# Optimization experiments

Measured on AMD Instinct MI355X. Metric: run time of the kernel, lower is better.

Reference implementation:

```python
import jax, jax.numpy as jnp
import numpy as np

# --- Mamba2Enc config (matches init_kwargs + mamba_ssm Mamba2 defaults) ---
D_IN = 1024
D_MODEL = 512
N_CLASSES = 2
NLAYERS = 2
D_STATE = 64
D_CONV = 4
EXPAND = 2
HEADDIM = 64
D_INNER = EXPAND * D_MODEL            # 1024
NHEADS = D_INNER // HEADDIM           # 16
CONV_DIM = D_INNER + 2 * D_STATE      # 1152 (ngroups=1)
D_IN_PROJ = 2 * D_INNER + 2 * D_STATE + NHEADS  # 2192
EPS = 1e-5


def setup_inputs() -> dict:
    key = jax.random.key(0)
    ks = jax.random.split(key, 10)
    def w(k, shape, sc=0.02):
        return jax.random.normal(k, shape, jnp.float32) * sc
    x = jax.random.normal(ks[0], (4, 4096, D_IN), jnp.float32)
    # fc1
    W1 = w(ks[1], (D_MODEL, D_IN))
    b1 = jnp.zeros((D_MODEL,), jnp.float32)
    # per-layer params stacked on leading NLAYERS axis
    ln_w = jnp.ones((NLAYERS, D_MODEL), jnp.float32)
    ln_b = jnp.zeros((NLAYERS, D_MODEL), jnp.float32)
    W_in = w(ks[2], (NLAYERS, D_IN_PROJ, D_MODEL))
    conv_w = w(ks[3], (NLAYERS, CONV_DIM, D_CONV), 0.1)
    conv_b = jnp.zeros((NLAYERS, CONV_DIM), jnp.float32)
    # dt_bias so that softplus(dt_bias) ~ [0.001, 0.1] (mamba init range)
    dt_bias = jax.random.uniform(ks[4], (NLAYERS, NHEADS), jnp.float32, -6.0, -2.3)
    A_log = jnp.log(jnp.tile(jnp.arange(1, NHEADS + 1, dtype=jnp.float32), (NLAYERS, 1)))
    Dskip = jnp.ones((NLAYERS, NHEADS), jnp.float32)
    norm_w = jnp.ones((NLAYERS, D_INNER), jnp.float32)
    W_out = w(ks[5], (NLAYERS, D_MODEL, D_INNER))
    # classifier
    Wc = w(ks[6], (N_CLASSES, D_MODEL))
    bc = jnp.zeros((N_CLASSES,), jnp.float32)
    return dict(x=x, W1=W1, b1=b1, ln_w=ln_w, ln_b=ln_b, W_in=W_in,
                conv_w=conv_w, conv_b=conv_b, dt_bias=dt_bias, A_log=A_log,
                Dskip=Dskip, norm_w=norm_w, W_out=W_out, Wc=Wc, bc=bc)


def _layernorm(h, w, b):
    mu = jnp.mean(h, axis=-1, keepdims=True)
    var = jnp.mean(jnp.square(h - mu), axis=-1, keepdims=True)
    return (h - mu) * jax.lax.rsqrt(var + EPS) * w + b


def _silu(x):
    return x * jax.nn.sigmoid(x)


def _mamba2(x, W_in, conv_w, conv_b, dt_bias, A_log, Dskip, norm_w, W_out):
    b, l, _ = x.shape
    zxbcdt = jnp.einsum('bld,ed->ble', x, W_in)  # (b, l, D_IN_PROJ)
    z = zxbcdt[..., :D_INNER]
    xBC = zxbcdt[..., D_INNER:D_INNER + CONV_DIM]
    dt = jax.nn.softplus(zxbcdt[..., -NHEADS:] + dt_bias)  # (b, l, h)
    # causal depthwise conv1d (kernel D_CONV) + silu
    xp = jnp.pad(xBC, ((0, 0), (D_CONV - 1, 0), (0, 0)))
    xBC = sum(xp[:, k:k + l, :] * conv_w[:, k] for k in range(D_CONV)) + conv_b
    xBC = _silu(xBC)
    xh = xBC[..., :D_INNER].reshape(b, l, NHEADS, HEADDIM)
    B = xBC[..., D_INNER:D_INNER + D_STATE]   # (b, l, n) ngroups=1
    C = xBC[..., D_INNER + D_STATE:]          # (b, l, n)
    A = -jnp.exp(A_log)                       # (h,)
    dA = jnp.exp(dt * A)                      # (b, l, h)
    dtx = dt[..., None] * xh                  # (b, l, h, p)

    def step(hstate, inp):
        dA_t, dtx_t, B_t, C_t = inp  # (b,h), (b,h,p), (b,n), (b,n)
        hstate = hstate * dA_t[:, :, None, None] + dtx_t[:, :, None, :] * B_t[:, None, :, None]
        y = jnp.einsum('bn,bhnp->bhp', C_t, hstate)
        return hstate, y

    init = jnp.zeros((b, NHEADS, D_STATE, HEADDIM), x.dtype)
    xs = (dA.transpose(1, 0, 2), dtx.transpose(1, 0, 2, 3),
          B.transpose(1, 0, 2), C.transpose(1, 0, 2))
    _, ys = jax.lax.scan(step, init, xs)      # ys: (l, b, h, p)
    y = ys.transpose(1, 0, 2, 3) + Dskip[None, None, :, None] * xh
    y = y.reshape(b, l, D_INNER)
    # RMSNormGated (norm_before_gate=False): rmsnorm(y * silu(z)) * weight
    y = y * _silu(z)
    y = y * jax.lax.rsqrt(jnp.mean(jnp.square(y), axis=-1, keepdims=True) + EPS) * norm_w
    return jnp.einsum('ble,de->bld', y, W_out)


def reference(x, W1, b1, ln_w, ln_b, W_in, conv_w, conv_b, dt_bias, A_log,
              Dskip, norm_w, W_out, Wc, bc):
    # fc1: Linear + GELU (dropout is identity at eval)
    h = jax.nn.gelu(jnp.einsum('bli,di->bld', x, W1) + b1, approximate=False)
    for i in range(NLAYERS):
        h = h + _mamba2(_layernorm(h, ln_w[i], ln_b[i]), W_in[i], conv_w[i],
                        conv_b[i], dt_bias[i], A_log[i], Dskip[i], norm_w[i], W_out[i])
    return jnp.einsum('bld,cd->blc', h, Wc) + bc
```

## Files before the change

kernel.cpp:

```cpp
#include <hip/hip_runtime.h>
#include <hip/hip_bf16.h>
#include <math.h>

#define BATCH 4
#define SEQ 4096
#define ROWS 16384
#define DIN 1024
#define DMODEL 512
#define DINNER 1024
#define DSTATE 64
#define NH 16
#define HD 64
#define CONVDIM 1152
#define DPROJ 2192
#define NPAD 2304
#define QC 64
#define NCH 64
#define LD 72

typedef __attribute__((ext_vector_type(8))) __bf16 bf16x8;
typedef __attribute__((ext_vector_type(4))) __bf16 bf16x4;
typedef __attribute__((ext_vector_type(4))) float f32x4;

__device__ __forceinline__ float siluf(float x){ return x / (1.f + __expf(-x)); }
__device__ __forceinline__ float geluf(float x){ return 0.5f*x*(1.f + erff(x*0.70710678118654752440f)); }

__device__ __forceinline__ bf16x8 scale8(bf16x8 v, float s){
  bf16x8 r;
  #pragma unroll
  for (int e = 0; e < 8; e++) r[e] = (__bf16)((float)v[e]*s);
  return r;
}

__global__ void cast_bf16_kernel(const float* __restrict__ src, __bf16* __restrict__ dst, long n){
  long i = (long)blockIdx.x*blockDim.x + threadIdx.x;
  long stride = (long)gridDim.x*blockDim.x;
  for (; i < n; i += stride) dst[i] = (__bf16)src[i];
}

__global__ void pad_win_kernel(const float* __restrict__ src, __bf16* __restrict__ dst){
  long total = 2L*NPAD*DMODEL;
  long i = (long)blockIdx.x*blockDim.x + threadIdx.x;
  long stride = (long)gridDim.x*blockDim.x;
  for (; i < total; i += stride){
    int k = (int)(i % DMODEL);
    int n = (int)((i / DMODEL) % NPAD);
    int l = (int)(i / ((long)DMODEL*NPAD));
    float v = (n < DPROJ) ? src[((long)l*DPROJ + n)*DMODEL + k] : 0.f;
    dst[i] = (__bf16)v;
  }
}

template<typename OutT, int EPI>
__global__ __launch_bounds__(256) void gemm_bt(const __bf16* __restrict__ A, const __bf16* __restrict__ Bm,
                                               OutT* __restrict__ C, const float* __restrict__ bias,
                                               int K, int Nc){
  __shared__ __align__(16) __bf16 As[128*32];
  __shared__ __align__(16) __bf16 Bs[128*32];
  int bm = blockIdx.x, bn = blockIdx.y;
  int tid = threadIdx.x;
  int lane = tid & 63, wid = tid >> 6;
  int wm = (wid >> 1)*64, wn = (wid & 1)*64;
  int lr = lane & 15, kb = lane >> 4;
  f32x4 acc[4][4] = {};
  const char* Ab = (const char*)A + (size_t)bm*128*(size_t)(K*2);
  const char* Bb = (const char*)Bm + (size_t)bn*128*(size_t)(K*2);
  int nkk = K >> 5;
  for (int kk = 0; kk < nkk; kk++){
    #pragma unroll
    for (int it = 0; it < 2; it++){
      int off = it*4096 + tid*16;
      int row = off >> 6, cb = off & 63;
      *(int4*)((char*)As + off) = *(const int4*)(Ab + (size_t)row*(K*2) + kk*64 + cb);
      *(int4*)((char*)Bs + off) = *(const int4*)(Bb + (size_t)row*(K*2) + kk*64 + cb);
    }
    __syncthreads();
    bf16x8 af[4], bfr[4];
    #pragma unroll
    for (int mi = 0; mi < 4; mi++) af[mi] = *(const bf16x8*)(As + (wm + mi*16 + lr)*32 + kb*8);
    #pragma unroll
    for (int ni = 0; ni < 4; ni++) bfr[ni] = *(const bf16x8*)(Bs + (wn + ni*16 + lr)*32 + kb*8);
    #pragma unroll
    for (int mi = 0; mi < 4; mi++)
      #pragma unroll
      for (int ni = 0; ni < 4; ni++)
        acc[mi][ni] = __builtin_amdgcn_mfma_f32_16x16x32_bf16(af[mi], bfr[ni], acc[mi][ni], 0, 0, 0);
    __syncthreads();
  }
  #pragma unroll
  for (int mi = 0; mi < 4; mi++){
    #pragma unroll
    for (int ni = 0; ni < 4; ni++){
      int r0 = bm*128 + wm + mi*16 + (lane >> 4)*4;
      int c  = bn*128 + wn + ni*16 + lr;
      if (c < Nc){
        OutT* Cp = C + (size_t)r0*Nc + c;
        #pragma unroll
        for (int j = 0; j < 4; j++){
          float v = acc[mi][ni][j];
          if (EPI == 1){ float u = v + bias[c]; v = geluf(u); }
          if (EPI == 2){ v += (float)Cp[(size_t)j*Nc]; }
          Cp[(size_t)j*Nc] = (OutT)v;
        }
      }
    }
  }
}

__global__ __launch_bounds__(256) void ln_kernel(const float* __restrict__ h, const float* __restrict__ w,
                                                 const float* __restrict__ b, __bf16* __restrict__ out){
  int row = blockIdx.x*4 + (threadIdx.x >> 6);
  int lane = threadIdx.x & 63;
  const float* hr = h + (size_t)row*DMODEL + lane*8;
  float4 a = *(const float4*)hr, a2 = *(const float4*)(hr+4);
  float v[8] = {a.x,a.y,a.z,a.w,a2.x,a2.y,a2.z,a2.w};
  float s = 0.f;
  #pragma unroll
  for (int i = 0; i < 8; i++) s += v[i];
  #pragma unroll
  for (int o = 32; o; o >>= 1) s += __shfl_xor(s, o, 64);
  float mu = s*(1.f/512.f);
  float q = 0.f;
  #pragma unroll
  for (int i = 0; i < 8; i++){ float d = v[i]-mu; q += d*d; }
  #pragma unroll
  for (int o = 32; o; o >>= 1) q += __shfl_xor(q, o, 64);
  float rs = rsqrtf(q*(1.f/512.f) + 1e-5f);
  const float* wp = w + lane*8; const float* bp = b + lane*8;
  bf16x8 o8;
  #pragma unroll
  for (int i = 0; i < 8; i++) o8[i] = (__bf16)((v[i]-mu)*rs*wp[i] + bp[i]);
  *(bf16x8*)(out + (size_t)row*DMODEL + lane*8) = o8;
}

__global__ __launch_bounds__(256) void conv_bc(const __bf16* __restrict__ zx, const float* __restrict__ cw,
                                               const float* __restrict__ cb, float* __restrict__ BCc){
  int idx = blockIdx.x*256 + threadIdx.x;
  int j = idx & 127;
  long bt = idx >> 7;
  int t = (int)(bt & (SEQ-1));
  int ch = DINNER + j;
  const __bf16* src = zx + (size_t)bt*DPROJ + 2048 + j;
  float acc = cb[ch] + (float)src[0]*cw[ch*4+3];
  if (t >= 1) acc += (float)src[-1L*DPROJ]*cw[ch*4+2];
  if (t >= 2) acc += (float)src[-2L*DPROJ]*cw[ch*4+1];
  if (t >= 3) acc += (float)src[-3L*DPROJ]*cw[ch*4+0];
  BCc[idx] = siluf(acc);
}

__global__ __launch_bounds__(256) void dt_kernel(const __bf16* __restrict__ zx, const float* __restrict__ dt_bias,
                                                 float* __restrict__ dtb){
  int idx = blockIdx.x*256 + threadIdx.x;
  int hh = idx & (NH-1); long bt = idx >> 4;
  float v = (float)zx[(size_t)bt*DPROJ + (DPROJ-NH) + hh] + dt_bias[hh];
  dtb[idx] = (v > 20.f) ? v : log1pf(__expf(v));
}

__global__ __launch_bounds__(64) void ssd_state(const __bf16* __restrict__ zx, const float* __restrict__ BCc,
                                                const float* __restrict__ dtb, const float* __restrict__ A_log,
                                                const float* __restrict__ cw, const float* __restrict__ cb,
                                                __bf16* __restrict__ Schunk, float* __restrict__ Pbuf){
  __shared__ __align__(16) __bf16 Bt[64*LD];
  __shared__ __align__(16) __bf16 Xt[64*LD];
  int c = blockIdx.x, h = blockIdx.y, b = blockIdx.z;
  int lane = threadIdx.x;
  int lr = lane & 15, kb = lane >> 4, hi4 = lane >> 4;
  long t0 = (long)c*QC;
  size_t bt0 = (size_t)b*SEQ + t0;
  int bh = b*NH + h;
  float Ac = -expf(A_log[h]);
  float dtv = dtb[(bt0 + lane)*NH + h];
  float cum = dtv*Ac;
  #pragma unroll
  for (int off = 1; off < 64; off <<= 1){ float v = __shfl_up(cum, off, 64); if (lane >= off) cum += v; }
  float cumQ = __shfl(cum, 63, 64);
  float w = __expf(cumQ - cum) * dtv;
  {
    const float* bp = BCc + bt0*128 + lane;
    for (int tb = 0; tb < 8; tb++){
      bf16x8 buf;
      #pragma unroll
      for (int u = 0; u < 8; u++){
        int t = tb*8 + u;
        float bv = bp[(size_t)t*128];
        float wt = __shfl(w, t, 64);
        buf[u] = (__bf16)(bv*wt);
      }
      *(bf16x8*)&Bt[lane*LD + tb*8] = buf;
    }
  }
  {
    int ch = h*HD + lane;
    float w0 = cw[ch*4], w1 = cw[ch*4+1], w2 = cw[ch*4+2], w3 = cw[ch*4+3], cbv = cb[ch];
    const __bf16* xp = zx + bt0*DPROJ + (DINNER + ch);
    float x1 = (t0 >= 1) ? (float)xp[-1L*DPROJ] : 0.f;
    float x2 = (t0 >= 2) ? (float)xp[-2L*DPROJ] : 0.f;
    float x3 = (t0 >= 3) ? (float)xp[-3L*DPROJ] : 0.f;
    for (int tb = 0; tb < 8; tb++){
      bf16x8 buf;
      #pragma unroll
      for (int u = 0; u < 8; u++){
        int t = tb*8 + u;
        float x0 = (float)xp[(size_t)t*DPROJ];
        float xv = siluf(cbv + w3*x0 + w2*x1 + w1*x2 + w0*x3);
        x3 = x2; x2 = x1; x1 = x0;
        buf[u] = (__bf16)xv;
      }
      *(bf16x8*)&Xt[lane*LD + tb*8] = buf;
    }
  }
  f32x4 acc[4][4] = {};
  #pragma unroll
  for (int kk = 0; kk < 2; kk++){
    bf16x8 af[4], bfr[4];
    #pragma unroll
    for (int mi = 0; mi < 4; mi++) af[mi]  = *(bf16x8*)&Bt[(mi*16+lr)*LD + kk*32 + kb*8];
    #pragma unroll
    for (int ni = 0; ni < 4; ni++) bfr[ni] = *(bf16x8*)&Xt[(ni*16+lr)*LD + kk*32 + kb*8];
    #pragma unroll
    for (int mi = 0; mi < 4; mi++)
      #pragma unroll
      for (int ni = 0; ni < 4; ni++)
        acc[mi][ni] = __builtin_amdgcn_mfma_f32_16x16x32_bf16(af[mi], bfr[ni], acc[mi][ni], 0, 0, 0);
  }
  __bf16* Sp = Schunk + ((size_t)bh*NCH + c)*4096;
  #pragma unroll
  for (int mi = 0; mi < 4; mi++)
    #pragma unroll
    for (int ni = 0; ni < 4; ni++){
      int n0 = mi*16 + hi4*4;
      int p  = ni*16 + lr;
      bf16x4 v;
      #pragma unroll
      for (int r = 0; r < 4; r++) v[r] = (__bf16)acc[mi][ni][r];
      *(bf16x4*)&Sp[p*64 + n0] = v;
    }
  if (lane == 0) Pbuf[bh*NCH + c] = __expf(cumQ);
}

__global__ __launch_bounds__(64) void ssd_comb(__bf16* __restrict__ Schunk, const float* __restrict__ Pbuf){
  int bh = blockIdx.x >> 4;
  int eb = blockIdx.x & 15;
  int e = eb*256 + threadIdx.x*4;
  __bf16* base = Schunk + (size_t)bh*NCH*4096 + e;
  float T0 = 0.f, T1 = 0.f, T2 = 0.f, T3 = 0.f;
  for (int c = 0; c < NCH; c++){
    float P = Pbuf[bh*NCH + c];
    bf16x4* p = (bf16x4*)(base + (size_t)c*4096);
    bf16x4 s = *p;
    bf16x4 o; o[0] = (__bf16)T0; o[1] = (__bf16)T1; o[2] = (__bf16)T2; o[3] = (__bf16)T3;
    *p = o;
    T0 = T0*P + (float)s[0]; T1 = T1*P + (float)s[1];
    T2 = T2*P + (float)s[2]; T3 = T3*P + (float)s[3];
  }
}

__global__ __launch_bounds__(64) void ssd_y(const __bf16* __restrict__ zx, const float* __restrict__ BCc,
                                            const float* __restrict__ dtb, const float* __restrict__ A_log,
                                            const float* __restrict__ Dskip, const float* __restrict__ cw,
                                            const float* __restrict__ cb, const __bf16* __restrict__ Spre,
                                            __bf16* __restrict__ yout){
  __shared__ __align__(16) __bf16 BnG[64*LD];
  __shared__ __align__(16) __bf16 Cn[64*LD];
  __shared__ __align__(16) __bf16 Xt[64*LD];
  __shared__ float cum_s[64], dt_s[64];
  int c = blockIdx.x, h = blockIdx.y, b = blockIdx.z;
  int lane = threadIdx.x;
  int lr = lane & 15, kb = lane >> 4, hi4 = lane >> 4;
  long t0 = (long)c*QC;
  size_t bt0 = (size_t)b*SEQ + t0;
  int bh = b*NH + h;
  float Ac = -expf(A_log[h]);
  float Dk = Dskip[h];
  float dtv = dtb[(bt0 + lane)*NH + h];
  float cum = dtv*Ac;
  #pragma unroll
  for (int off = 1; off < 64; off <<= 1){ float v = __shfl_up(cum, off, 64); if (lane >= off) cum += v; }
  cum_s[lane] = cum; dt_s[lane] = dtv;
  for (int r = 0; r < 32; r++){
    int t = r*2 + (lane >> 5);
    int idx = (lane & 31)*4;
    float4 v = *(const float4*)&BCc[(bt0 + t)*128 + idx];
    bf16x4 bv; bv[0] = (__bf16)v.x; bv[1] = (__bf16)v.y; bv[2] = (__bf16)v.z; bv[3] = (__bf16)v.w;
    __bf16* dst = (idx < 64) ? &BnG[t*LD + idx] : &Cn[t*LD + (idx - 64)];
    *(bf16x4*)dst = bv;
  }
  {
    int ch = h*HD + lane;
    float w0 = cw[ch*4], w1 = cw[ch*4+1], w2 = cw[ch*4+2], w3 = cw[ch*4+3], cbv = cb[ch];
    const __bf16* xp = zx + bt0*DPROJ + (DINNER + ch);
    float x1 = (t0 >= 1) ? (float)xp[-1L*DPROJ] : 0.f;
    float x2 = (t0 >= 2) ? (float)xp[-2L*DPROJ] : 0.f;
    float x3 = (t0 >= 3) ? (float)xp[-3L*DPROJ] : 0.f;
    for (int tb = 0; tb < 8; tb++){
      bf16x8 buf;
      #pragma unroll
      for (int u = 0; u < 8; u++){
        int t = tb*8 + u;
        float x0 = (float)xp[(size_t)t*DPROJ];
        float xv = siluf(cbv + w3*x0 + w2*x1 + w1*x2 + w0*x3);
        x3 = x2; x2 = x1; x1 = x0;
        buf[u] = (__bf16)xv;
      }
      *(bf16x8*)&Xt[lane*LD + tb*8] = buf;
    }
  }
  bf16x8 cf[4][2];
  #pragma unroll
  for (int ni = 0; ni < 4; ni++)
    #pragma unroll
    for (int kk = 0; kk < 2; kk++)
      cf[ni][kk] = *(bf16x8*)&Cn[(ni*16+lr)*LD + kk*32 + kb*8];
  f32x4 g[4][4] = {};
  #pragma unroll
  for (int kk = 0; kk < 2; kk++){
    bf16x8 bfj[4];
    #pragma unroll
    for (int mi = 0; mi < 4; mi++) bfj[mi] = *(bf16x8*)&BnG[(mi*16+lr)*LD + kk*32 + kb*8];
    #pragma unroll
    for (int mi = 0; mi < 4; mi++)
      #pragma unroll
      for (int ni = 0; ni < 4; ni++)
        g[mi][ni] = __builtin_amdgcn_mfma_f32_16x16x32_bf16(bfj[mi], cf[ni][kk], g[mi][ni], 0, 0, 0);
  }
  float cumi[4];
  #pragma unroll
  for (int ni = 0; ni < 4; ni++) cumi[ni] = cum_s[ni*16 + lr];
  #pragma unroll
  for (int mi = 0; mi < 4; mi++){
    #pragma unroll
    for (int r = 0; r < 4; r++){
      int j = mi*16 + hi4*4 + r;
      float cj = cum_s[j], dj = dt_s[j];
      #pragma unroll
      for (int ni = 0; ni < 4; ni++){
        int i = ni*16 + lr;
        float v = g[mi][ni][r];
        if (i > j)       v = v * __expf(cumi[ni] - cj) * dj;
        else if (i == j) v = v*dj + Dk;
        else             v = 0.f;
        g[mi][ni][r] = v;
      }
    }
  }
  #pragma unroll
  for (int mi = 0; mi < 4; mi++)
    #pragma unroll
    for (int ni = 0; ni < 4; ni++){
      int j0 = mi*16 + hi4*4;
      int i  = ni*16 + lr;
      bf16x4 v;
      #pragma unroll
      for (int r = 0; r < 4; r++) v[r] = (__bf16)g[mi][ni][r];
      *(bf16x4*)&BnG[i*LD + j0] = v;
    }
  f32x4 y4[4][4] = {};
  #pragma unroll
  for (int kk = 0; kk < 2; kk++){
    bf16x8 af2[4], bf2[4];
    #pragma unroll
    for (int mi = 0; mi < 4; mi++) af2[mi] = *(bf16x8*)&Xt[(mi*16+lr)*LD + kk*32 + kb*8];
    #pragma unroll
    for (int ni = 0; ni < 4; ni++) bf2[ni] = *(bf16x8*)&BnG[(ni*16+lr)*LD + kk*32 + kb*8];
    #pragma unroll
    for (int mi = 0; mi < 4; mi++)
      #pragma unroll
      for (int ni = 0; ni < 4; ni++)
        y4[mi][ni] = __builtin_amdgcn_mfma_f32_16x16x32_bf16(af2[mi], bf2[ni], y4[mi][ni], 0, 0, 0);
  }
  {
    const __bf16* Sp = Spre + ((size_t)bh*NCH + c)*4096;
    float ei[4];
    #pragma unroll
    for (int ni = 0; ni < 4; ni++) ei[ni] = __expf(cumi[ni]);
    #pragma unroll
    for (int kk = 0; kk < 2; kk++){
      bf16x8 as1[4];
      #pragma unroll
      for (int mi = 0; mi < 4; mi++) as1[mi] = *(const bf16x8*)&Sp[(mi*16+lr)*64 + kk*32 + kb*8];
      #pragma unroll
      for (int ni = 0; ni < 4; ni++){
        bf16x8 cs = scale8(cf[ni][kk], ei[ni]);
        #pragma unroll
        for (int mi = 0; mi < 4; mi++)
          y4[mi][ni] = __builtin_amdgcn_mfma_f32_16x16x32_bf16(as1[mi], cs, y4[mi][ni], 0, 0, 0);
      }
    }
  }
  #pragma unroll
  for (int mi = 0; mi < 4; mi++)
    #pragma unroll
    for (int ni = 0; ni < 4; ni++){
      int p0 = mi*16 + hi4*4;
      int i  = ni*16 + lr;
      bf16x4 v;
      #pragma unroll
      for (int r = 0; r < 4; r++) v[r] = (__bf16)y4[mi][ni][r];
      *(bf16x4*)&yout[(bt0 + i)*DINNER + h*HD + p0] = v;
    }
}

__global__ __launch_bounds__(256) void gate_rms(__bf16* __restrict__ y, const __bf16* __restrict__ zx,
                                                const float* __restrict__ nw){
  int row = blockIdx.x*4 + (threadIdx.x >> 6);
  int lane = threadIdx.x & 63;
  __bf16* yr = y + (size_t)row*DINNER + lane*16;
  const __bf16* zr = zx + (size_t)row*DPROJ + lane*16;
  bf16x8 y0 = *(const bf16x8*)yr, y1 = *(const bf16x8*)(yr+8);
  bf16x8 z0 = *(const bf16x8*)zr, z1 = *(const bf16x8*)(zr+8);
  float v[16]; float ss = 0.f;
  #pragma unroll
  for (int i = 0; i < 8; i++){ float z = (float)z0[i]; float tv = (float)y0[i]*siluf(z); v[i] = tv; ss += tv*tv; }
  #pragma unroll
  for (int i = 0; i < 8; i++){ float z = (float)z1[i]; float tv = (float)y1[i]*siluf(z); v[8+i] = tv; ss += tv*tv; }
  #pragma unroll
  for (int o = 32; o; o >>= 1) ss += __shfl_xor(ss, o, 64);
  float rs = rsqrtf(ss*(1.f/1024.f) + 1e-5f);
  const float* np = nw + lane*16;
  bf16x8 o0, o1;
  #pragma unroll
  for (int i = 0; i < 8; i++){ o0[i] = (__bf16)(v[i]*rs*np[i]); o1[i] = (__bf16)(v[8+i]*rs*np[8+i]); }
  *(bf16x8*)yr = o0; *(bf16x8*)(yr+8) = o1;
}

__global__ __launch_bounds__(256) void cls_kernel(const float* __restrict__ h, const float* __restrict__ Wc,
                                                  const float* __restrict__ bc, float* __restrict__ out){
  int row = blockIdx.x*4 + (threadIdx.x >> 6);
  int lane = threadIdx.x & 63;
  const float* hr = h + (size_t)row*DMODEL + lane*8;
  float4 a = *(const float4*)hr, a2 = *(const float4*)(hr+4);
  float hv[8] = {a.x,a.y,a.z,a.w,a2.x,a2.y,a2.z,a2.w};
  const float* w0 = Wc + lane*8;
  const float* w1 = Wc + DMODEL + lane*8;
  float s0 = 0.f, s1 = 0.f;
  #pragma unroll
  for (int i = 0; i < 8; i++){ s0 += hv[i]*w0[i]; s1 += hv[i]*w1[i]; }
  #pragma unroll
  for (int o = 32; o; o >>= 1){ s0 += __shfl_xor(s0, o, 64); s1 += __shfl_xor(s1, o, 64); }
  if (lane == 0){ out[(size_t)row*2] = s0 + bc[0]; out[(size_t)row*2 + 1] = s1 + bc[1]; }
}

extern "C" void kernel_launch(void* const* d_in, const int* in_sizes, int n_in,
                              void* d_out, int out_size, void* d_ws, size_t ws_size,
                              hipStream_t stream){
  const float* x       = (const float*)d_in[0];
  const float* W1      = (const float*)d_in[1];
  const float* b1      = (const float*)d_in[2];
  const float* ln_w    = (const float*)d_in[3];
  const float* ln_b    = (const float*)d_in[4];
  const float* W_in    = (const float*)d_in[5];
  const float* conv_w  = (const float*)d_in[6];
  const float* conv_b  = (const float*)d_in[7];
  const float* dt_bias = (const float*)d_in[8];
  const float* A_log   = (const float*)d_in[9];
  const float* Dskip   = (const float*)d_in[10];
  const float* norm_w  = (const float*)d_in[11];
  const float* W_out   = (const float*)d_in[12];
  const float* Wc      = (const float*)d_in[13];
  const float* bc      = (const float*)d_in[14];
  float* out = (float*)d_out;
  char* ws = (char*)d_ws;

  size_t off = 0;
  auto alloc = [&](size_t bytes){ void* p = ws + off; off += (bytes + 255) & ~(size_t)255; return p; };
  char*   regionA = (char*) alloc((size_t)ROWS*DIN*2);
  __bf16* W1b     = (__bf16*)alloc((size_t)DMODEL*DIN*2);
  __bf16* Winb    = (__bf16*)alloc(2L*NPAD*DMODEL*2);
  __bf16* Woutb   = (__bf16*)alloc(2L*DMODEL*DINNER*2);
  float*  h       = (float*) alloc((size_t)ROWS*DMODEL*4);
  __bf16* zx      = (__bf16*)alloc((size_t)ROWS*DPROJ*2);
  float*  BCc     = (float*) alloc((size_t)ROWS*128*4);
  float*  dtb     = (float*) alloc((size_t)ROWS*NH*4);
  __bf16* ybuf    = (__bf16*)alloc((size_t)ROWS*DINNER*2);
  float*  Pbuf    = (float*) alloc(64L*NCH*4);
  if (off > ws_size) return;

  __bf16* x_bf   = (__bf16*)regionA;
  __bf16* hnb    = (__bf16*)regionA;
  __bf16* Schunk = (__bf16*)regionA;

  cast_bf16_kernel<<<4096, 256, 0, stream>>>(x, x_bf, (long)ROWS*DIN);
  cast_bf16_kernel<<<512, 256, 0, stream>>>(W1, W1b, (long)DMODEL*DIN);
  cast_bf16_kernel<<<1024, 256, 0, stream>>>(W_out, Woutb, 2L*DMODEL*DINNER);
  pad_win_kernel<<<2048, 256, 0, stream>>>(W_in, Winb);

  {
    dim3 g(ROWS/128, DMODEL/128);
    gemm_bt<float,1><<<g, 256, 0, stream>>>(x_bf, W1b, h, b1, DIN, DMODEL);
  }

  for (int l = 0; l < 2; l++){
    ln_kernel<<<ROWS/4, 256, 0, stream>>>(h, ln_w + l*DMODEL, ln_b + l*DMODEL, hnb);
    {
      dim3 g(ROWS/128, NPAD/128);
      gemm_bt<__bf16,0><<<g, 256, 0, stream>>>(hnb, Winb + (size_t)l*NPAD*DMODEL, zx, nullptr, DMODEL, DPROJ);
    }
    conv_bc<<<(ROWS*128)/256, 256, 0, stream>>>(zx, conv_w + l*CONVDIM*4, conv_b + l*CONVDIM, BCc);
    dt_kernel<<<(ROWS*NH)/256, 256, 0, stream>>>(zx, dt_bias + l*NH, dtb);
    {
      dim3 g(NCH, NH, BATCH);
      ssd_state<<<g, 64, 0, stream>>>(zx, BCc, dtb, A_log + l*NH,
                                      conv_w + l*CONVDIM*4, conv_b + l*CONVDIM, Schunk, Pbuf);
      ssd_comb<<<64*16, 64, 0, stream>>>(Schunk, Pbuf);
      ssd_y<<<g, 64, 0, stream>>>(zx, BCc, dtb, A_log + l*NH, Dskip + l*NH,
                                  conv_w + l*CONVDIM*4, conv_b + l*CONVDIM, Schunk, ybuf);
    }
    gate_rms<<<ROWS/4, 256, 0, stream>>>(ybuf, zx, norm_w + l*DINNER);
    {
      dim3 g(ROWS/128, DMODEL/128);
      gemm_bt<float,2><<<g, 256, 0, stream>>>(ybuf, Woutb + (size_t)l*DMODEL*DINNER, h, nullptr, DINNER, DMODEL);
    }
  }

  cls_kernel<<<ROWS/4, 256, 0, stream>>>(h, Wc, bc, out);
}
```

Before: 571.3 us.

## Use direct-to-LDS GEMM loads, bf16 BC buffer, transposed dt, reuse conv output in SSD

The GEMM tile loads now go through global_load_lds, which writes global memory straight into LDS without staging in registers. The conv'd B/C buffer is stored in bf16 instead of fp32, and dt is written head-major so each chunk reads it contiguously. ssd_state writes the conv+silu x values to a new xhT buffer so ssd_y no longer recomputes the convolution, and ssd_y reads B/C fragments directly from global memory. Both SSD kernels now pack several chunks per block as separate waves. The cost is an extra ROWS×DINNER bf16 buffer and one more global write per element.

```diff
diff --git a/kernel.cpp b/kernel.cpp
--- a/kernel.cpp
+++ b/kernel.cpp
@@ -30,6 +30,11 @@
   #pragma unroll
   for (int e = 0; e < 8; e++) r[e] = (__bf16)((float)v[e]*s);
   return r;
+}
+
+__device__ __forceinline__ void gl_lds16(const void* g, void* l){
+  __builtin_amdgcn_global_load_lds((const __attribute__((address_space(1))) void*)g,
+                                   (__attribute__((address_space(3))) void*)l, 16, 0, 0);
 }
 
 __global__ void cast_bf16_kernel(const float* __restrict__ src, __bf16* __restrict__ dst, long n){
@@ -69,10 +74,11 @@
   for (int kk = 0; kk < nkk; kk++){
     #pragma unroll
     for (int it = 0; it < 2; it++){
-      int off = it*4096 + tid*16;
+      int base = it*4096 + wid*1024;
+      int off  = base + lane*16;
       int row = off >> 6, cb = off & 63;
-      *(int4*)((char*)As + off) = *(const int4*)(Ab + (size_t)row*(K*2) + kk*64 + cb);
-      *(int4*)((char*)Bs + off) = *(const int4*)(Bb + (size_t)row*(K*2) + kk*64 + cb);
+      gl_lds16(Ab + (size_t)row*(K*2) + kk*64 + cb, (char*)As + base);
+      gl_lds16(Bb + (size_t)row*(K*2) + kk*64 + cb, (char*)Bs + base);
     }
     __syncthreads();
     bf16x8 af[4], bfr[4];
@@ -134,7 +140,7 @@
 }
 
 __global__ __launch_bounds__(256) void conv_bc(const __bf16* __restrict__ zx, const float* __restrict__ cw,
-                                               const float* __restrict__ cb, float* __restrict__ BCc){
+                                               const float* __restrict__ cb, __bf16* __restrict__ BCc){
   int idx = blockIdx.x*256 + threadIdx.x;
   int j = idx & 127;
   long bt = idx >> 7;
@@ -145,46 +151,50 @@
   if (t >= 1) acc += (float)src[-1L*DPROJ]*cw[ch*4+2];
   if (t >= 2) acc += (float)src[-2L*DPROJ]*cw[ch*4+1];
   if (t >= 3) acc += (float)src[-3L*DPROJ]*cw[ch*4+0];
-  BCc[idx] = siluf(acc);
+  BCc[idx] = (__bf16)siluf(acc);
 }
 
 __global__ __launch_bounds__(256) void dt_kernel(const __bf16* __restrict__ zx, const float* __restrict__ dt_bias,
-                                                 float* __restrict__ dtb){
+                                                 float* __restrict__ dtT){
   int idx = blockIdx.x*256 + threadIdx.x;
   int hh = idx & (NH-1); long bt = idx >> 4;
+  int b = (int)(bt >> 12); int t = (int)(bt & (SEQ-1));
   float v = (float)zx[(size_t)bt*DPROJ + (DPROJ-NH) + hh] + dt_bias[hh];
-  dtb[idx] = (v > 20.f) ? v : log1pf(__expf(v));
-}
-
-__global__ __launch_bounds__(64) void ssd_state(const __bf16* __restrict__ zx, const float* __restrict__ BCc,
-                                                const float* __restrict__ dtb, const float* __restrict__ A_log,
-                                                const float* __restrict__ cw, const float* __restrict__ cb,
-                                                __bf16* __restrict__ Schunk, float* __restrict__ Pbuf){
-  __shared__ __align__(16) __bf16 Bt[64*LD];
-  __shared__ __align__(16) __bf16 Xt[64*LD];
-  int c = blockIdx.x, h = blockIdx.y, b = blockIdx.z;
-  int lane = threadIdx.x;
+  float sp = (v > 20.f) ? v : log1pf(__expf(v));
+  dtT[((size_t)b*NH + hh)*SEQ + t] = sp;
+}
+
+__global__ __launch_bounds__(128) void ssd_state(const __bf16* __restrict__ zx, const __bf16* __restrict__ BCc,
+                                                 const float* __restrict__ dtT, const float* __restrict__ A_log,
+                                                 const float* __restrict__ cw, const float* __restrict__ cb,
+                                                 __bf16* __restrict__ Schunk, float* __restrict__ Pbuf,
+                                                 __bf16* __restrict__ xhT){
+  __shared__ __align__(16) __bf16 Bt_all[2][64*LD];
+  __shared__ __align__(16) __bf16 Xt_all[2][64*LD];
+  int widx = threadIdx.x >> 6, lane = threadIdx.x & 63;
+  int c = blockIdx.x*2 + widx, h = blockIdx.y, b = blockIdx.z;
+  __bf16* Bt = Bt_all[widx];
+  __bf16* Xt = Xt_all[widx];
   int lr = lane & 15, kb = lane >> 4, hi4 = lane >> 4;
   long t0 = (long)c*QC;
   size_t bt0 = (size_t)b*SEQ + t0;
   int bh = b*NH + h;
   float Ac = -expf(A_log[h]);
-  float dtv = dtb[(bt0 + lane)*NH + h];
+  float dtv = dtT[(size_t)bh*SEQ + t0 + lane];
   float cum = dtv*Ac;
   #pragma unroll
   for (int off = 1; off < 64; off <<= 1){ float v = __shfl_up(cum, off, 64); if (lane >= off) cum += v; }
   float cumQ = __shfl(cum, 63, 64);
   float w = __expf(cumQ - cum) * dtv;
   {
-    const float* bp = BCc + bt0*128 + lane;
+    const __bf16* bp = BCc + bt0*128 + lane;
     for (int tb = 0; tb < 8; tb++){
       bf16x8 buf;
       #pragma unroll
       for (int u = 0; u < 8; u++){
         int t = tb*8 + u;
-        float bv = bp[(size_t)t*128];
-        float wt = __shfl(w, t, 64);
-        buf[u] = (__bf16)(bv*wt);
+        float bv = (float)bp[(size_t)t*128];
+        buf[u] = (__bf16)(bv * __shfl(w, t, 64));
       }
       *(bf16x8*)&Bt[lane*LD + tb*8] = buf;
     }
@@ -196,6 +206,7 @@
     float x1 = (t0 >= 1) ? (float)xp[-1L*DPROJ] : 0.f;
     float x2 = (t0 >= 2) ? (float)xp[-2L*DPROJ] : 0.f;
     float x3 = (t0 >= 3) ? (float)xp[-3L*DPROJ] : 0.f;
+    __bf16* xo = xhT + ((size_t)bh*NCH + c)*4096 + lane*64;
     for (int tb = 0; tb < 8; tb++){
       bf16x8 buf;
       #pragma unroll
@@ -207,6 +218,7 @@
         buf[u] = (__bf16)xv;
       }
       *(bf16x8*)&Xt[lane*LD + tb*8] = buf;
+      *(bf16x8*)(xo + tb*8) = buf;
     }
   }
   f32x4 acc[4][4] = {};
@@ -255,68 +267,40 @@
   }
 }
 
-__global__ __launch_bounds__(64) void ssd_y(const __bf16* __restrict__ zx, const float* __restrict__ BCc,
-                                            const float* __restrict__ dtb, const float* __restrict__ A_log,
-                                            const float* __restrict__ Dskip, const float* __restrict__ cw,
-                                            const float* __restrict__ cb, const __bf16* __restrict__ Spre,
-                                            __bf16* __restrict__ yout){
-  __shared__ __align__(16) __bf16 BnG[64*LD];
-  __shared__ __align__(16) __bf16 Cn[64*LD];
-  __shared__ __align__(16) __bf16 Xt[64*LD];
-  __shared__ float cum_s[64], dt_s[64];
-  int c = blockIdx.x, h = blockIdx.y, b = blockIdx.z;
-  int lane = threadIdx.x;
+__global__ __launch_bounds__(256) void ssd_y(const __bf16* __restrict__ BCc, const float* __restrict__ dtT,
+                                             const float* __restrict__ A_log, const float* __restrict__ Dskip,
+                                             const __bf16* __restrict__ xhT, const __bf16* __restrict__ Spre,
+                                             __bf16* __restrict__ yout){
+  __shared__ __align__(16) __bf16 Gs_all[4][64*LD];
+  __shared__ float cum_all[4][64], dt_all[4][64];
+  int widx = threadIdx.x >> 6, lane = threadIdx.x & 63;
+  int c = blockIdx.x*4 + widx, h = blockIdx.y, b = blockIdx.z;
+  __bf16* Gs = Gs_all[widx];
+  float* cum_s = cum_all[widx];
+  float* dt_s = dt_all[widx];
   int lr = lane & 15, kb = lane >> 4, hi4 = lane >> 4;
   long t0 = (long)c*QC;
   size_t bt0 = (size_t)b*SEQ + t0;
   int bh = b*NH + h;
   float Ac = -expf(A_log[h]);
   float Dk = Dskip[h];
-  float dtv = dtb[(bt0 + lane)*NH + h];
+  float dtv = dtT[(size_t)bh*SEQ + t0 + lane];
   float cum = dtv*Ac;
   #pragma unroll
   for (int off = 1; off < 64; off <<= 1){ float v = __shfl_up(cum, off, 64); if (lane >= off) cum += v; }
   cum_s[lane] = cum; dt_s[lane] = dtv;
-  for (int r = 0; r < 32; r++){
-    int t = r*2 + (lane >> 5);
-    int idx = (lane & 31)*4;
-    float4 v = *(const float4*)&BCc[(bt0 + t)*128 + idx];
-    bf16x4 bv; bv[0] = (__bf16)v.x; bv[1] = (__bf16)v.y; bv[2] = (__bf16)v.z; bv[3] = (__bf16)v.w;
-    __bf16* dst = (idx < 64) ? &BnG[t*LD + idx] : &Cn[t*LD + (idx - 64)];
-    *(bf16x4*)dst = bv;
-  }
-  {
-    int ch = h*HD + lane;
-    float w0 = cw[ch*4], w1 = cw[ch*4+1], w2 = cw[ch*4+2], w3 = cw[ch*4+3], cbv = cb[ch];
-    const __bf16* xp = zx + bt0*DPROJ + (DINNER + ch);
-    float x1 = (t0 >= 1) ? (float)xp[-1L*DPROJ] : 0.f;
-    float x2 = (t0 >= 2) ? (float)xp[-2L*DPROJ] : 0.f;
-    float x3 = (t0 >= 3) ? (float)xp[-3L*DPROJ] : 0.f;
-    for (int tb = 0; tb < 8; tb++){
-      bf16x8 buf;
-      #pragma unroll
-      for (int u = 0; u < 8; u++){
-        int t = tb*8 + u;
-        float x0 = (float)xp[(size_t)t*DPROJ];
-        float xv = siluf(cbv + w3*x0 + w2*x1 + w1*x2 + w0*x3);
-        x3 = x2; x2 = x1; x1 = x0;
-        buf[u] = (__bf16)xv;
-      }
-      *(bf16x8*)&Xt[lane*LD + tb*8] = buf;
-    }
-  }
   bf16x8 cf[4][2];
   #pragma unroll
   for (int ni = 0; ni < 4; ni++)
     #pragma unroll
     for (int kk = 0; kk < 2; kk++)
-      cf[ni][kk] = *(bf16x8*)&Cn[(ni*16+lr)*LD + kk*32 + kb*8];
+      cf[ni][kk] = *(const bf16x8*)&BCc[(bt0 + ni*16 + lr)*128 + 64 + kk*32 + kb*8];
   f32x4 g[4][4] = {};
   #pragma unroll
   for (int kk = 0; kk < 2; kk++){
     bf16x8 bfj[4];
     #pragma unroll
-    for (int mi = 0; mi < 4; mi++) bfj[mi] = *(bf16x8*)&BnG[(mi*16+lr)*LD + kk*32 + kb*8];
+    for (int mi = 0; mi < 4; mi++) bfj[mi] = *(const bf16x8*)&BCc[(bt0 + mi*16 + lr)*128 + kk*32 + kb*8];
     #pragma unroll
     for (int mi = 0; mi < 4; mi++)
       #pragma unroll
@@ -352,16 +336,17 @@
       bf16x4 v;
       #pragma unroll
       for (int r = 0; r < 4; r++) v[r] = (__bf16)g[mi][ni][r];
-      *(bf16x4*)&BnG[i*LD + j0] = v;
-    }
+      *(bf16x4*)&Gs[i*LD + j0] = v;
+    }
+  const __bf16* Xp = xhT + ((size_t)bh*NCH + c)*4096;
   f32x4 y4[4][4] = {};
   #pragma unroll
   for (int kk = 0; kk < 2; kk++){
     bf16x8 af2[4], bf2[4];
     #pragma unroll
-    for (int mi = 0; mi < 4; mi++) af2[mi] = *(bf16x8*)&Xt[(mi*16+lr)*LD + kk*32 + kb*8];
-    #pragma unroll
-    for (int ni = 0; ni < 4; ni++) bf2[ni] = *(bf16x8*)&BnG[(ni*16+lr)*LD + kk*32 + kb*8];
+    for (int mi = 0; mi < 4; mi++) af2[mi] = *(const bf16x8*)&Xp[(mi*16+lr)*64 + kk*32 + kb*8];
+    #pragma unroll
+    for (int ni = 0; ni < 4; ni++) bf2[ni] = *(bf16x8*)&Gs[(ni*16+lr)*LD + kk*32 + kb*8];
     #pragma unroll
     for (int mi = 0; mi < 4; mi++)
       #pragma unroll
@@ -469,9 +454,10 @@
   __bf16* Woutb   = (__bf16*)alloc(2L*DMODEL*DINNER*2);
   float*  h       = (float*) alloc((size_t)ROWS*DMODEL*4);
   __bf16* zx      = (__bf16*)alloc((size_t)ROWS*DPROJ*2);
-  float*  BCc     = (float*) alloc((size_t)ROWS*128*4);
-  float*  dtb     = (float*) alloc((size_t)ROWS*NH*4);
+  __bf16* BCc     = (__bf16*)alloc((size_t)ROWS*128*2);
+  float*  dtT     = (float*) alloc((size_t)ROWS*NH*4);
   __bf16* ybuf    = (__bf16*)alloc((size_t)ROWS*DINNER*2);
+  __bf16* xhT     = (__bf16*)alloc((size_t)ROWS*DINNER*2);
   float*  Pbuf    = (float*) alloc(64L*NCH*4);
   if (off > ws_size) return;
 
@@ -496,14 +482,14 @@
       gemm_bt<__bf16,0><<<g, 256, 0, stream>>>(hnb, Winb + (size_t)l*NPAD*DMODEL, zx, nullptr, DMODEL, DPROJ);
     }
     conv_bc<<<(ROWS*128)/256, 256, 0, stream>>>(zx, conv_w + l*CONVDIM*4, conv_b + l*CONVDIM, BCc);
-    dt_kernel<<<(ROWS*NH)/256, 256, 0, stream>>>(zx, dt_bias + l*NH, dtb);
+    dt_kernel<<<(ROWS*NH)/256, 256, 0, stream>>>(zx, dt_bias + l*NH, dtT);
     {
-      dim3 g(NCH, NH, BATCH);
-      ssd_state<<<g, 64, 0, stream>>>(zx, BCc, dtb, A_log + l*NH,
-                                      conv_w + l*CONVDIM*4, conv_b + l*CONVDIM, Schunk, Pbuf);
+      dim3 gs(NCH/2, NH, BATCH);
+      ssd_state<<<gs, 128, 0, stream>>>(zx, BCc, dtT, A_log + l*NH,
+                                        conv_w + l*CONVDIM*4, conv_b + l*CONVDIM, Schunk, Pbuf, xhT);
       ssd_comb<<<64*16, 64, 0, stream>>>(Schunk, Pbuf);
-      ssd_y<<<g, 64, 0, stream>>>(zx, BCc, dtb, A_log + l*NH, Dskip + l*NH,
-                                  conv_w + l*CONVDIM*4, conv_b + l*CONVDIM, Schunk, ybuf);
+      dim3 gy(NCH/4, NH, BATCH);
+      ssd_y<<<gy, 256, 0, stream>>>(BCc, dtT, A_log + l*NH, Dskip + l*NH, xhT, Schunk, ybuf);
     }
     gate_rms<<<ROWS/4, 256, 0, stream>>>(ybuf, zx, norm_w + l*DINNER);
     {
```

Measured after the change: 529.4 us. -7.3%, faster.
